# Performance work log

Measured on AMD Instinct MI355X. Metric: run time of the kernel, lower is better.

Reference implementation:

```python
import jax, jax.numpy as jnp
import numpy as np

WH, WW = 7, 7
N_HEADS = 6
INPUT_DIM = 192
HEAD_DIM = INPUT_DIM // N_HEADS
QK_SCALE = HEAD_DIM ** (-0.5)


def _relative_position_index(wh, ww):
    coords = np.stack(np.meshgrid(np.arange(wh), np.arange(ww), indexing='ij'))  # (2, wh, ww)
    cf = coords.reshape(2, -1)                       # (2, N)
    rel = cf[:, :, None] - cf[:, None, :]            # (2, N, N)
    rel = rel.transpose(1, 2, 0).copy()              # (N, N, 2)
    rel[:, :, 0] += wh - 1
    rel[:, :, 1] += ww - 1
    rel[:, :, 0] *= 2 * ww - 1
    return jnp.asarray(rel.sum(-1), dtype=jnp.int32)  # (N, N)

_REL_IDX = _relative_position_index(WH, WW)


def setup_inputs() -> dict:
    key = jax.random.key(0)
    ks = jax.random.split(key, 7)
    bW, nW = 4096, 64
    N = WH * WW
    s = 0.02
    return {
        "x": jax.random.normal(ks[0], (bW, WH, WW, INPUT_DIM), jnp.float32),
        "mask": jax.random.normal(ks[1], (nW, N, N), jnp.float32),
        "qkv_w": jax.random.normal(ks[2], (3 * INPUT_DIM, INPUT_DIM), jnp.float32) * s,
        "qkv_b": jax.random.normal(ks[3], (3 * INPUT_DIM,), jnp.float32) * s,
        "out_w": jax.random.normal(ks[4], (INPUT_DIM, INPUT_DIM), jnp.float32) * s,
        "out_b": jax.random.normal(ks[5], (INPUT_DIM,), jnp.float32) * s,
        "rpb_table": jax.random.normal(ks[6], ((2 * WH - 1) * (2 * WW - 1), N_HEADS), jnp.float32) * s,
    }


def reference(x, mask, qkv_w, qkv_b, out_w, out_b, rpb_table):
    b, Wh, Ww, C = x.shape
    N = Wh * Ww
    H, D = N_HEADS, HEAD_DIM
    # 1x1 conv == pointwise linear over channels-last input
    qkv = jnp.einsum('bxyc,oc->bxyo', x, qkv_w) + qkv_b          # (b, Wh, Ww, 3C)
    qkv = qkv.reshape(b, N, 3, H, D)                             # chunk order q,k,v; (h d) channel layout
    q, k, v = qkv[:, :, 0], qkv[:, :, 1], qkv[:, :, 2]           # (b, N, H, D)
    q = q * QK_SCALE
    sim = jnp.einsum('bihd,bjhd->bhij', q, k)                    # (b, H, N, N)
    # relative position bias gather
    rpb = rpb_table[_REL_IDX]                                    # (N, N, H)
    sim = sim + rpb.transpose(2, 0, 1)[None]                     # + (1, H, N, N)
    # shift mask add over windows
    nW = mask.shape[0]
    sim = sim.reshape(b // nW, nW, H, N, N) + mask[None, :, None]
    attn = jax.nn.softmax(sim, axis=-1).reshape(b, H, N, N)
    out = jnp.einsum('bhij,bjhd->bihd', attn, v)                 # (b, N, H, D)
    out = out.reshape(b, N, H * D)                               # (h d) channel order
    out = jnp.einsum('bnc,oc->bno', out, out_w) + out_b
    return out.reshape(b, Wh, Ww, C)
```

## Files before the change

### kernel.cpp

```cpp
#include <hip/hip_runtime.h>
#include <hip/hip_bf16.h>

typedef __bf16 bf16;
typedef __bf16 bf16x4 __attribute__((ext_vector_type(4)));
typedef __bf16 bf16x8 __attribute__((ext_vector_type(8)));
typedef float f32x4 __attribute__((ext_vector_type(4)));
typedef float floatv4 __attribute__((ext_vector_type(4)));

#define QK_SCALE 0.17677669529663687f

#define X_LD 200
#define QK_LD 40
#define VT_LD 72

__device__ __forceinline__ bf16* x_ptr(bf16* base, int row, int col) {
    return base + row * X_LD + col;
}
__device__ __forceinline__ bf16* qk_ptr(bf16* base, int row, int col) {
    return base + row * QK_LD + col;
}
__device__ __forceinline__ bf16* vt_ptr(bf16* base, int row, int col) {
    return base + row * VT_LD + col;
}

__global__ void wmsa_prep(const float* __restrict__ qkv_w,
                          const float* __restrict__ out_w,
                          const float* __restrict__ rpb_table,
                          const float* __restrict__ mask,
                          bf16* __restrict__ qkv_wb,
                          bf16* __restrict__ out_wb,
                          float* __restrict__ rpbx,
                          float* __restrict__ combo,
                          int build_combo) {
    int t = blockIdx.x * 256 + threadIdx.x;
    if (t < 110592) qkv_wb[t] = (bf16)qkv_w[t];
    if (t < 36864)  out_wb[t] = (bf16)out_w[t];
    if (t < 14406) {
        int h = t / 2401, ij = t % 2401, i = ij / 49, j = ij % 49;
        int ri = (i / 7 - j / 7 + 6) * 13 + (i % 7 - j % 7 + 6);
        rpbx[t] = rpb_table[ri * 6 + h];
    }
    if (build_combo && t < 64 * 6 * 64 * 64) {
        int j = t & 63, i = (t >> 6) & 63, r = t >> 12;
        int h = r % 6, w = r / 6;
        float v = -1e30f;
        if (i < 49 && j < 49) {
            int ri = (i / 7 - j / 7 + 6) * 13 + (i % 7 - j % 7 + 6);
            v = rpb_table[ri * 6 + h] + mask[w * 2401 + i * 49 + j];
        }
        combo[t] = v;
    }
}

template <bool USE_COMBO>
__global__ __launch_bounds__(768, 3) void wmsa_fused(
    const float* __restrict__ x, const float* __restrict__ mask,
    const float* __restrict__ qkv_b, const float* __restrict__ out_b,
    const bf16* __restrict__ qkv_wb, const bf16* __restrict__ out_wb,
    const float* __restrict__ rpbx, const float* __restrict__ combo,
    float* __restrict__ out)
{
    __shared__ __align__(16) bf16 s_x[64 * X_LD];
    __shared__ __align__(16) bf16 s_qp[6][64 * QK_LD];
    __shared__ __align__(16) bf16 s_k[6][64 * QK_LD];
    __shared__ __align__(16) bf16 s_vt[6][32 * VT_LD];

    const int b    = blockIdx.x;
    const int tid  = threadIdx.x;
    const int wv   = tid >> 6;
    const int lane = tid & 63;
    const int lo   = lane & 15;
    const int hi   = lane >> 4;

    const float* xw    = x + (size_t)b * 9408;
    const int    obase = wv * 48;
    const int    sec   = wv >> 2;

    {
        const int c0 = tid;
        const int r0s = c0 / 24, cc0 = c0 % 24;
        const float* p0 = xw + r0s * 192 + cc0 * 8;
        floatv4 f0 = *(const floatv4*)p0;
        floatv4 f1 = *(const floatv4*)(p0 + 4);
        bf16x8 v;
        v[0]=(bf16)f0[0]; v[1]=(bf16)f0[1]; v[2]=(bf16)f0[2]; v[3]=(bf16)f0[3];
        v[4]=(bf16)f1[0]; v[5]=(bf16)f1[1]; v[6]=(bf16)f1[2]; v[7]=(bf16)f1[3];
        *(bf16x8*)&s_x[r0s * X_LD + cc0 * 8] = v;

        const int c1 = tid + 768;
        const int r1s = c1 / 24, cc1 = c1 % 24;
        bf16x8 w = {};
        if (r1s < 49) {
            const float* p1 = xw + r1s * 192 + cc1 * 8;
            floatv4 g0 = *(const floatv4*)p1;
            floatv4 g1 = *(const floatv4*)(p1 + 4);
            w[0]=(bf16)g0[0]; w[1]=(bf16)g0[1]; w[2]=(bf16)g0[2]; w[3]=(bf16)g0[3];
            w[4]=(bf16)g1[0]; w[5]=(bf16)g1[1]; w[6]=(bf16)g1[2]; w[7]=(bf16)g1[3];
        }
        *(bf16x8*)&s_x[r1s * X_LD + cc1 * 8] = w;
    }
    __syncthreads();

#pragma unroll 1
    for (int mib = 0; mib < 2; ++mib) {
        f32x4 acc[2][3];
#pragma unroll
        for (int mi = 0; mi < 2; ++mi)
#pragma unroll
            for (int nj = 0; nj < 3; ++nj) acc[mi][nj] = (f32x4){0.f, 0.f, 0.f, 0.f};

        const int r0 = mib * 32 + lo;
        const int r1 = r0 + 16;

        auto loadB = [&](bf16x8* dst, int kk) {
#pragma unroll
            for (int nj = 0; nj < 3; ++nj)
                dst[nj] = *(const bf16x8*)(qkv_wb + (obase + nj * 16 + lo) * 192 + kk * 32 + hi * 8);
        };

        bf16x8 b0_[3], b1_[3], b2_[3];
        loadB(b0_, 0);
        loadB(b1_, 1);
#pragma unroll
        for (int kk = 0; kk < 6; ++kk) {
            if (kk < 4) loadB(b2_, kk + 2);
            bf16x8 a0 = *(const bf16x8*)x_ptr(s_x, r0, kk * 32 + hi * 8);
            bf16x8 a1 = *(const bf16x8*)x_ptr(s_x, r1, kk * 32 + hi * 8);
            acc[0][0] = __builtin_amdgcn_mfma_f32_16x16x32_bf16(a0, b0_[0], acc[0][0], 0, 0, 0);
            acc[1][0] = __builtin_amdgcn_mfma_f32_16x16x32_bf16(a1, b0_[0], acc[1][0], 0, 0, 0);
            acc[0][1] = __builtin_amdgcn_mfma_f32_16x16x32_bf16(a0, b0_[1], acc[0][1], 0, 0, 0);
            acc[1][1] = __builtin_amdgcn_mfma_f32_16x16x32_bf16(a1, b0_[1], acc[1][1], 0, 0, 0);
            acc[0][2] = __builtin_amdgcn_mfma_f32_16x16x32_bf16(a0, b0_[2], acc[0][2], 0, 0, 0);
            acc[1][2] = __builtin_amdgcn_mfma_f32_16x16x32_bf16(a1, b0_[2], acc[1][2], 0, 0, 0);
            b0_[0] = b1_[0]; b0_[1] = b1_[1]; b0_[2] = b1_[2];
            b1_[0] = b2_[0]; b1_[1] = b2_[1]; b1_[2] = b2_[2];
        }

        if (sec < 2) {
#pragma unroll
            for (int nj = 0; nj < 3; ++nj) {
                const int o    = obase + nj * 16 + lo;
                const float bs = qkv_b[o];
                const int oc   = o - sec * 192;
                const int hh   = oc >> 5;
                const int dd   = oc & 31;
                bf16* base = (sec == 0) ? &s_qp[hh][0] : &s_k[hh][0];
#pragma unroll
                for (int mi = 0; mi < 2; ++mi)
#pragma unroll
                    for (int r = 0; r < 4; ++r) {
                        const int n = mib * 32 + mi * 16 + hi * 4 + r;
                        const float v = acc[mi][nj][r] + bs;
                        *qk_ptr(base, n, dd) = (sec == 0) ? (bf16)(v * QK_SCALE) : (bf16)v;
                    }
            }
        } else {
#pragma unroll
            for (int nj = 0; nj < 3; ++nj) {
                const int o    = obase + nj * 16 + lo;
                const float bs = qkv_b[o];
                const int oc   = o - 384;
                const int hh   = oc >> 5;
                const int dd   = oc & 31;
#pragma unroll
                for (int mi = 0; mi < 2; ++mi) {
                    const int n0 = mib * 32 + mi * 16 + hi * 4;
                    bf16x4 pk;
#pragma unroll
                    for (int r = 0; r < 4; ++r) pk[r] = (bf16)(acc[mi][nj][r] + bs);
                    *(bf16x4*)vt_ptr(&s_vt[hh][0], dd, n0) = pk;
                }
            }
        }
    }
    __syncthreads();

    {
        const int h    = wv >> 1;
        const int arow = (wv & 1) * 32;
        bf16* qb    = &s_qp[h][0];
        bf16* kbase = &s_k[h][0];

        f32x4 cv[2][4];
        if (USE_COMBO) {
            const float* cb = combo + (((size_t)(b & 63) * 6 + h) << 12);
#pragma unroll
            for (int mi = 0; mi < 2; ++mi) {
                const int i = arow + mi * 16 + lo;
#pragma unroll
                for (int nt = 0; nt < 4; ++nt)
                    cv[mi][nt] = *(const floatv4*)(cb + i * 64 + nt * 16 + hi * 4);
            }
        }

        bf16x8 qa0 = *(const bf16x8*)qk_ptr(qb, arow + lo, hi * 8);
        bf16x8 qa1 = *(const bf16x8*)qk_ptr(qb, arow + 16 + lo, hi * 8);
        bf16x8 kb0 = *(const bf16x8*)qk_ptr(kbase,  0 + lo, hi * 8);
        bf16x8 kb1 = *(const bf16x8*)qk_ptr(kbase, 16 + lo, hi * 8);
        bf16x8 kb2 = *(const bf16x8*)qk_ptr(kbase, 32 + lo, hi * 8);
        bf16x8 kb3 = *(const bf16x8*)qk_ptr(kbase, 48 + lo, hi * 8);

        f32x4 t[4][2];
#pragma unroll
        for (int nt = 0; nt < 4; ++nt)
#pragma unroll
            for (int mi = 0; mi < 2; ++mi) t[nt][mi] = (f32x4){0.f, 0.f, 0.f, 0.f};
        t[0][0] = __builtin_amdgcn_mfma_f32_16x16x32_bf16(kb0, qa0, t[0][0], 0, 0, 0);
        t[1][0] = __builtin_amdgcn_mfma_f32_16x16x32_bf16(kb1, qa0, t[1][0], 0, 0, 0);
        t[2][0] = __builtin_amdgcn_mfma_f32_16x16x32_bf16(kb2, qa0, t[2][0], 0, 0, 0);
        t[3][0] = __builtin_amdgcn_mfma_f32_16x16x32_bf16(kb3, qa0, t[3][0], 0, 0, 0);
        t[0][1] = __builtin_amdgcn_mfma_f32_16x16x32_bf16(kb0, qa1, t[0][1], 0, 0, 0);
        t[1][1] = __builtin_amdgcn_mfma_f32_16x16x32_bf16(kb1, qa1, t[1][1], 0, 0, 0);
        t[2][1] = __builtin_amdgcn_mfma_f32_16x16x32_bf16(kb2, qa1, t[2][1], 0, 0, 0);
        t[3][1] = __builtin_amdgcn_mfma_f32_16x16x32_bf16(kb3, qa1, t[3][1], 0, 0, 0);

        if (USE_COMBO) {
#pragma unroll
            for (int mi = 0; mi < 2; ++mi)
#pragma unroll
                for (int nt = 0; nt < 4; ++nt) t[nt][mi] += cv[mi][nt];
        } else {
            const float* mk = mask + (size_t)(b & 63) * 2401;
            const float* rb = rpbx + h * 2401;
#pragma unroll
            for (int nt = 0; nt < 4; ++nt)
#pragma unroll
                for (int mi = 0; mi < 2; ++mi)
#pragma unroll
                    for (int r = 0; r < 4; ++r) {
                        const int i = arow + mi * 16 + lo;
                        const int j = nt * 16 + hi * 4 + r;
                        float sv = t[nt][mi][r];
                        if (j >= 49 || i >= 49) sv = -1e30f;
                        else sv += rb[i * 49 + j] + mk[i * 49 + j];
                        t[nt][mi][r] = sv;
                    }
        }

#pragma unroll
        for (int mi = 0; mi < 2; ++mi) {
            float m = t[0][mi][0];
#pragma unroll
            for (int nt = 0; nt < 4; ++nt)
#pragma unroll
                for (int r = 0; r < 4; ++r) m = fmaxf(m, t[nt][mi][r]);
            m = fmaxf(m, __shfl_xor(m, 16));
            m = fmaxf(m, __shfl_xor(m, 32));
            float sum = 0.f;
#pragma unroll
            for (int nt = 0; nt < 4; ++nt)
#pragma unroll
                for (int r = 0; r < 4; ++r) {
                    float pv = __expf(t[nt][mi][r] - m);
                    t[nt][mi][r] = pv;
                    sum += pv;
                }
            sum += __shfl_xor(sum, 16);
            sum += __shfl_xor(sum, 32);
            const float inv = 1.0f / sum;
#pragma unroll
            for (int nt = 0; nt < 4; ++nt)
#pragma unroll
                for (int r = 0; r < 4; ++r) t[nt][mi][r] *= inv;
        }

        f32x4 o00 = (f32x4){0.f,0.f,0.f,0.f}, o01 = (f32x4){0.f,0.f,0.f,0.f};
        f32x4 o10 = (f32x4){0.f,0.f,0.f,0.f}, o11 = (f32x4){0.f,0.f,0.f,0.f};
#pragma unroll
        for (int kk = 0; kk < 2; ++kk) {
#pragma unroll
            for (int mi = 0; mi < 2; ++mi)
#pragma unroll
                for (int c = 0; c < 2; ++c) {
                    const int nt = kk * 2 + c;
                    bf16x4 pk;
#pragma unroll
                    for (int r = 0; r < 4; ++r) pk[r] = (bf16)t[nt][mi][r];
                    *(bf16x4*)qk_ptr(qb, arow + mi * 16 + lo, c * 16 + hi * 4) = pk;
                }
            bf16x8 pa0 = *(const bf16x8*)qk_ptr(qb, arow + lo, hi * 8);
            bf16x8 pa1 = *(const bf16x8*)qk_ptr(qb, arow + 16 + lo, hi * 8);
            bf16x8 vb0 = *(const bf16x8*)vt_ptr(&s_vt[h][0],  0 + lo, kk * 32 + hi * 8);
            bf16x8 vb1 = *(const bf16x8*)vt_ptr(&s_vt[h][0], 16 + lo, kk * 32 + hi * 8);
            o00 = __builtin_amdgcn_mfma_f32_16x16x32_bf16(vb0, pa0, o00, 0, 0, 0);
            o01 = __builtin_amdgcn_mfma_f32_16x16x32_bf16(vb0, pa1, o01, 0, 0, 0);
            o10 = __builtin_amdgcn_mfma_f32_16x16x32_bf16(vb1, pa0, o10, 0, 0, 0);
            o11 = __builtin_amdgcn_mfma_f32_16x16x32_bf16(vb1, pa1, o11, 0, 0, 0);
        }

        {
            bf16x4 w00, w01, w10, w11;
#pragma unroll
            for (int r = 0; r < 4; ++r) {
                w00[r] = (bf16)o00[r]; w01[r] = (bf16)o01[r];
                w10[r] = (bf16)o10[r]; w11[r] = (bf16)o11[r];
            }
            *(bf16x4*)x_ptr(s_x, arow +  0 + lo, h * 32 +  0 + hi * 4) = w00;
            *(bf16x4*)x_ptr(s_x, arow + 16 + lo, h * 32 +  0 + hi * 4) = w01;
            *(bf16x4*)x_ptr(s_x, arow +  0 + lo, h * 32 + 16 + hi * 4) = w10;
            *(bf16x4*)x_ptr(s_x, arow + 16 + lo, h * 32 + 16 + hi * 4) = w11;
        }
    }
    __syncthreads();

    {
        const int o2 = wv * 16 + lo;
        f32x4 facc[4];
#pragma unroll
        for (int mi = 0; mi < 4; ++mi) facc[mi] = (f32x4){0.f, 0.f, 0.f, 0.f};

        bf16x8 fbc = *(const bf16x8*)(out_wb + o2 * 192 + hi * 8);
#pragma unroll
        for (int kk = 0; kk < 6; ++kk) {
            bf16x8 fbn;
            if (kk < 5) fbn = *(const bf16x8*)(out_wb + o2 * 192 + (kk + 1) * 32 + hi * 8);
            bf16x8 fa[4];
#pragma unroll
            for (int mi = 0; mi < 4; ++mi)
                fa[mi] = *(const bf16x8*)x_ptr(s_x, mi * 16 + lo, kk * 32 + hi * 8);
#pragma unroll
            for (int mi = 0; mi < 4; ++mi)
                facc[mi] = __builtin_amdgcn_mfma_f32_16x16x32_bf16(fa[mi], fbc, facc[mi], 0, 0, 0);
            fbc = fbn;
        }

        const float ob = out_b[o2];
        float* ow = out + (size_t)b * 9408;
#pragma unroll
        for (int mi = 0; mi < 4; ++mi)
#pragma unroll
            for (int r = 0; r < 4; ++r) {
                const int n = mi * 16 + hi * 4 + r;
                if (n < 49) ow[n * 192 + o2] = facc[mi][r] + ob;
            }
    }
}

extern "C" void kernel_launch(void* const* d_in, const int* in_sizes, int n_in,
                              void* d_out, int out_size, void* d_ws, size_t ws_size,
                              hipStream_t stream) {
    const float* x      = (const float*)d_in[0];
    const float* mask   = (const float*)d_in[1];
    const float* qkv_w  = (const float*)d_in[2];
    const float* qkv_b  = (const float*)d_in[3];
    const float* out_w  = (const float*)d_in[4];
    const float* out_b  = (const float*)d_in[5];
    const float* rpb    = (const float*)d_in[6];
    float* out          = (float*)d_out;

    char* ws = (char*)d_ws;
    bf16*  qkv_wb = (bf16*)ws;
    bf16*  out_wb = (bf16*)(ws + 221184);
    float* rpbx   = (float*)(ws + 294912);
    float* combo  = (float*)(ws + 352768);
    const bool use_combo = ws_size >= (size_t)(352768 + 6291456);

    hipLaunchKernelGGL(wmsa_prep, dim3(6144), dim3(256), 0, stream,
                       qkv_w, out_w, rpb, mask, qkv_wb, out_wb, rpbx, combo,
                       use_combo ? 1 : 0);
    if (use_combo)
        hipLaunchKernelGGL(HIP_KERNEL_NAME(wmsa_fused<true>), dim3(4096), dim3(768), 0, stream,
                           x, mask, qkv_b, out_b, qkv_wb, out_wb, rpbx, combo, out);
    else
        hipLaunchKernelGGL(HIP_KERNEL_NAME(wmsa_fused<false>), dim3(4096), dim3(768), 0, stream,
                           x, mask, qkv_b, out_b, qkv_wb, out_wb, rpbx, combo, out);
}
```

Measured before the change: 257.7 us.

## Halve block to 384 threads with compact swizzled LDS to fit more blocks

New measurement: 323.8 us. 1.26x slower.

```diff
diff --git a/kernel.cpp b/kernel.cpp
--- a/kernel.cpp
+++ b/kernel.cpp
@@ -9,18 +9,14 @@
 
 #define QK_SCALE 0.17677669529663687f
 
-#define X_LD 200
-#define QK_LD 40
-#define VT_LD 72
-
-__device__ __forceinline__ bf16* x_ptr(bf16* base, int row, int col) {
-    return base + row * X_LD + col;
+__device__ __forceinline__ bf16* t192_ptr(bf16* base, int row, int col) {
+    return base + row * 192 + ((((col >> 3) ^ (row & 7)) << 3)) + (col & 7);
 }
 __device__ __forceinline__ bf16* qk_ptr(bf16* base, int row, int col) {
-    return base + row * QK_LD + col;
+    return base + row * 32 + ((((col >> 3) ^ ((row >> 1) & 3)) << 3)) + (col & 7);
 }
 __device__ __forceinline__ bf16* vt_ptr(bf16* base, int row, int col) {
-    return base + row * VT_LD + col;
+    return base + row * 56 + col;
 }
 
 __global__ void wmsa_prep(const float* __restrict__ qkv_w,
@@ -53,17 +49,18 @@
 }
 
 template <bool USE_COMBO>
-__global__ __launch_bounds__(768, 3) void wmsa_fused(
+__global__ __launch_bounds__(384, 3) void wmsa_fused(
     const float* __restrict__ x, const float* __restrict__ mask,
     const float* __restrict__ qkv_b, const float* __restrict__ out_b,
     const bf16* __restrict__ qkv_wb, const bf16* __restrict__ out_wb,
     const float* __restrict__ rpbx, const float* __restrict__ combo,
     float* __restrict__ out)
 {
-    __shared__ __align__(16) bf16 s_x[64 * X_LD];
-    __shared__ __align__(16) bf16 s_qp[6][64 * QK_LD];
-    __shared__ __align__(16) bf16 s_k[6][64 * QK_LD];
-    __shared__ __align__(16) bf16 s_vt[6][32 * VT_LD];
+    __shared__ __align__(16) bf16 s_lds[39360];
+    bf16* s_x  = s_lds;
+    bf16* s_q  = s_lds + 9408;
+    bf16* s_k  = s_lds + 19008;
+    bf16* s_vt = s_lds + 28608;
 
     const int b    = blockIdx.x;
     const int tid  = threadIdx.x;
@@ -72,239 +69,247 @@
     const int lo   = lane & 15;
     const int hi   = lane >> 4;
 
-    const float* xw    = x + (size_t)b * 9408;
-    const int    obase = wv * 48;
-    const int    sec   = wv >> 2;
+    const float* xw  = x + (size_t)b * 9408;
+    const int    sec = wv >> 1;
+
+#pragma unroll
+    for (int q2 = 0; q2 < 4; ++q2) {
+        const int gc = q2 * 384 + tid;
+        if (gc < 1176) {
+            const int rs = gc / 24, cc = gc % 24;
+            const float* p = xw + rs * 192 + cc * 8;
+            floatv4 f0 = *(const floatv4*)p;
+            floatv4 f1 = *(const floatv4*)(p + 4);
+            bf16x8 v;
+            v[0]=(bf16)f0[0]; v[1]=(bf16)f0[1]; v[2]=(bf16)f0[2]; v[3]=(bf16)f0[3];
+            v[4]=(bf16)f1[0]; v[5]=(bf16)f1[1]; v[6]=(bf16)f1[2]; v[7]=(bf16)f1[3];
+            *(bf16x8*)&s_x[(rs * 24 + (cc ^ (rs & 7))) * 8] = v;
+        }
+    }
+    __syncthreads();
+
+#pragma unroll 1
+    for (int nj2 = 0; nj2 < 2; ++nj2) {
+        const int colbase = wv * 96 + nj2 * 48;
+#pragma unroll 1
+        for (int mib = 0; mib < 2; ++mib) {
+            f32x4 acc[2][3];
+#pragma unroll
+            for (int mi = 0; mi < 2; ++mi)
+#pragma unroll
+                for (int nj = 0; nj < 3; ++nj) acc[mi][nj] = (f32x4){0.f, 0.f, 0.f, 0.f};
+
+            const int r0 = mib * 32 + lo;
+            const int r1 = min(r0 + 16, 48);
+
+            auto loadB = [&](bf16x8* dst, int kk) {
+#pragma unroll
+                for (int nj = 0; nj < 3; ++nj)
+                    dst[nj] = *(const bf16x8*)(qkv_wb + (colbase + nj * 16 + lo) * 192 + kk * 32 + hi * 8);
+            };
+
+            bf16x8 b0_[3], b1_[3], b2_[3];
+            loadB(b0_, 0);
+            loadB(b1_, 1);
+#pragma unroll
+            for (int kk = 0; kk < 6; ++kk) {
+                if (kk < 4) loadB(b2_, kk + 2);
+                bf16x8 a0 = *(const bf16x8*)t192_ptr(s_x, r0, kk * 32 + hi * 8);
+                bf16x8 a1 = *(const bf16x8*)t192_ptr(s_x, r1, kk * 32 + hi * 8);
+                acc[0][0] = __builtin_amdgcn_mfma_f32_16x16x32_bf16(a0, b0_[0], acc[0][0], 0, 0, 0);
+                acc[1][0] = __builtin_amdgcn_mfma_f32_16x16x32_bf16(a1, b0_[0], acc[1][0], 0, 0, 0);
+                acc[0][1] = __builtin_amdgcn_mfma_f32_16x16x32_bf16(a0, b0_[1], acc[0][1], 0, 0, 0);
+                acc[1][1] = __builtin_amdgcn_mfma_f32_16x16x32_bf16(a1, b0_[1], acc[1][1], 0, 0, 0);
+                acc[0][2] = __builtin_amdgcn_mfma_f32_16x16x32_bf16(a0, b0_[2], acc[0][2], 0, 0, 0);
+                acc[1][2] = __builtin_amdgcn_mfma_f32_16x16x32_bf16(a1, b0_[2], acc[1][2], 0, 0, 0);
+                b0_[0] = b1_[0]; b0_[1] = b1_[1]; b0_[2] = b1_[2];
+                b1_[0] = b2_[0]; b1_[1] = b2_[1]; b1_[2] = b2_[2];
+            }
+
+            if (sec < 2) {
+#pragma unroll
+                for (int nj = 0; nj < 3; ++nj) {
+                    const int o    = colbase + nj * 16 + lo;
+                    const float bs = qkv_b[o];
+                    const int oc   = o - sec * 192;
+                    const int hh   = oc >> 5;
+                    const int dd   = oc & 31;
+                    bf16* base = (sec == 0) ? (s_q + hh * 1600) : (s_k + hh * 1600);
+#pragma unroll
+                    for (int mi = 0; mi < 2; ++mi)
+#pragma unroll
+                        for (int r = 0; r < 4; ++r) {
+                            const int n  = mib * 32 + mi * 16 + hi * 4 + r;
+                            const int nc = min(n, 49);
+                            const float v = acc[mi][nj][r] + bs;
+                            *qk_ptr(base, nc, dd) = (sec == 0) ? (bf16)(v * QK_SCALE) : (bf16)v;
+                        }
+                }
+            } else {
+#pragma unroll
+                for (int nj = 0; nj < 3; ++nj) {
+                    const int o    = colbase + nj * 16 + lo;
+                    const float bs = qkv_b[o];
+                    const int oc   = o - 384;
+                    const int hh   = oc >> 5;
+                    const int dd   = oc & 31;
+#pragma unroll
+                    for (int mi = 0; mi < 2; ++mi) {
+                        const int n0 = mib * 32 + mi * 16 + hi * 4;
+                        if (n0 < 56) {
+                            bf16x4 pk;
+#pragma unroll
+                            for (int r = 0; r < 4; ++r) pk[r] = (bf16)(acc[mi][nj][r] + bs);
+                            *(bf16x4*)vt_ptr(s_vt + hh * 1792, dd, n0) = pk;
+                        }
+                    }
+                }
+            }
+        }
+    }
+    __syncthreads();
 
     {
-        const int c0 = tid;
-        const int r0s = c0 / 24, cc0 = c0 % 24;
-        const float* p0 = xw + r0s * 192 + cc0 * 8;
-        floatv4 f0 = *(const floatv4*)p0;
-        floatv4 f1 = *(const floatv4*)(p0 + 4);
-        bf16x8 v;
-        v[0]=(bf16)f0[0]; v[1]=(bf16)f0[1]; v[2]=(bf16)f0[2]; v[3]=(bf16)f0[3];
-        v[4]=(bf16)f1[0]; v[5]=(bf16)f1[1]; v[6]=(bf16)f1[2]; v[7]=(bf16)f1[3];
-        *(bf16x8*)&s_x[r0s * X_LD + cc0 * 8] = v;
-
-        const int c1 = tid + 768;
-        const int r1s = c1 / 24, cc1 = c1 % 24;
-        bf16x8 w = {};
-        if (r1s < 49) {
-            const float* p1 = xw + r1s * 192 + cc1 * 8;
-            floatv4 g0 = *(const floatv4*)p1;
-            floatv4 g1 = *(const floatv4*)(p1 + 4);
-            w[0]=(bf16)g0[0]; w[1]=(bf16)g0[1]; w[2]=(bf16)g0[2]; w[3]=(bf16)g0[3];
-            w[4]=(bf16)g1[0]; w[5]=(bf16)g1[1]; w[6]=(bf16)g1[2]; w[7]=(bf16)g1[3];
-        }
-        *(bf16x8*)&s_x[r1s * X_LD + cc1 * 8] = w;
+        const int h = wv;
+        bf16* qb    = s_q + h * 1600;
+        bf16* kbase = s_k + h * 1600;
+        bf16* vtb   = s_vt + h * 1792;
+
+#pragma unroll 1
+        for (int p = 0; p < 2; ++p) {
+            const int arow = p * 32;
+
+            f32x4 cv[2][4];
+            if (USE_COMBO) {
+                const float* cb = combo + (((size_t)(b & 63) * 6 + h) << 12);
+#pragma unroll
+                for (int mi = 0; mi < 2; ++mi) {
+                    const int i = arow + mi * 16 + lo;
+#pragma unroll
+                    for (int nt = 0; nt < 4; ++nt)
+                        cv[mi][nt] = *(const floatv4*)(cb + i * 64 + nt * 16 + hi * 4);
+                }
+            }
+
+            bf16x8 qa0 = *(const bf16x8*)qk_ptr(qb, arow + lo, hi * 8);
+            bf16x8 qa1 = *(const bf16x8*)qk_ptr(qb, min(arow + 16 + lo, 49), hi * 8);
+            bf16x8 kb0 = *(const bf16x8*)qk_ptr(kbase,  0 + lo, hi * 8);
+            bf16x8 kb1 = *(const bf16x8*)qk_ptr(kbase, 16 + lo, hi * 8);
+            bf16x8 kb2 = *(const bf16x8*)qk_ptr(kbase, 32 + lo, hi * 8);
+            bf16x8 kb3 = *(const bf16x8*)qk_ptr(kbase, min(48 + lo, 49), hi * 8);
+
+            f32x4 t[4][2];
+#pragma unroll
+            for (int nt = 0; nt < 4; ++nt)
+#pragma unroll
+                for (int mi = 0; mi < 2; ++mi) t[nt][mi] = (f32x4){0.f, 0.f, 0.f, 0.f};
+            t[0][0] = __builtin_amdgcn_mfma_f32_16x16x32_bf16(kb0, qa0, t[0][0], 0, 0, 0);
+            t[1][0] = __builtin_amdgcn_mfma_f32_16x16x32_bf16(kb1, qa0, t[1][0], 0, 0, 0);
+            t[2][0] = __builtin_amdgcn_mfma_f32_16x16x32_bf16(kb2, qa0, t[2][0], 0, 0, 0);
+            t[3][0] = __builtin_amdgcn_mfma_f32_16x16x32_bf16(kb3, qa0, t[3][0], 0, 0, 0);
+            t[0][1] = __builtin_amdgcn_mfma_f32_16x16x32_bf16(kb0, qa1, t[0][1], 0, 0, 0);
+            t[1][1] = __builtin_amdgcn_mfma_f32_16x16x32_bf16(kb1, qa1, t[1][1], 0, 0, 0);
+            t[2][1] = __builtin_amdgcn_mfma_f32_16x16x32_bf16(kb2, qa1, t[2][1], 0, 0, 0);
+            t[3][1] = __builtin_amdgcn_mfma_f32_16x16x32_bf16(kb3, qa1, t[3][1], 0, 0, 0);
+
+            if (USE_COMBO) {
+#pragma unroll
+                for (int mi = 0; mi < 2; ++mi)
+#pragma unroll
+                    for (int nt = 0; nt < 4; ++nt) t[nt][mi] += cv[mi][nt];
+            } else {
+                const float* mk = mask + (size_t)(b & 63) * 2401;
+                const float* rb = rpbx + h * 2401;
+#pragma unroll
+                for (int nt = 0; nt < 4; ++nt)
+#pragma unroll
+                    for (int mi = 0; mi < 2; ++mi)
+#pragma unroll
+                        for (int r = 0; r < 4; ++r) {
+                            const int i = arow + mi * 16 + lo;
+                            const int j = nt * 16 + hi * 4 + r;
+                            float sv = t[nt][mi][r];
+                            if (j >= 49 || i >= 49) sv = -1e30f;
+                            else sv += rb[i * 49 + j] + mk[i * 49 + j];
+                            t[nt][mi][r] = sv;
+                        }
+            }
+
+#pragma unroll
+            for (int mi = 0; mi < 2; ++mi) {
+                float m = t[0][mi][0];
+#pragma unroll
+                for (int nt = 0; nt < 4; ++nt)
+#pragma unroll
+                    for (int r = 0; r < 4; ++r) m = fmaxf(m, t[nt][mi][r]);
+                m = fmaxf(m, __shfl_xor(m, 16));
+                m = fmaxf(m, __shfl_xor(m, 32));
+                float sum = 0.f;
+#pragma unroll
+                for (int nt = 0; nt < 4; ++nt)
+#pragma unroll
+                    for (int r = 0; r < 4; ++r) {
+                        float pv = __expf(t[nt][mi][r] - m);
+                        t[nt][mi][r] = pv;
+                        sum += pv;
+                    }
+                sum += __shfl_xor(sum, 16);
+                sum += __shfl_xor(sum, 32);
+                const float inv = 1.0f / sum;
+#pragma unroll
+                for (int nt = 0; nt < 4; ++nt)
+#pragma unroll
+                    for (int r = 0; r < 4; ++r) t[nt][mi][r] *= inv;
+            }
+
+            f32x4 o00 = (f32x4){0.f,0.f,0.f,0.f}, o01 = (f32x4){0.f,0.f,0.f,0.f};
+            f32x4 o10 = (f32x4){0.f,0.f,0.f,0.f}, o11 = (f32x4){0.f,0.f,0.f,0.f};
+#pragma unroll
+            for (int kk = 0; kk < 2; ++kk) {
+#pragma unroll
+                for (int mi = 0; mi < 2; ++mi)
+#pragma unroll
+                    for (int c = 0; c < 2; ++c) {
+                        const int nt = kk * 2 + c;
+                        bf16x4 pk;
+#pragma unroll
+                        for (int r = 0; r < 4; ++r) pk[r] = (bf16)t[nt][mi][r];
+                        *(bf16x4*)qk_ptr(qb, min(arow + mi * 16 + lo, 49), c * 16 + hi * 4) = pk;
+                    }
+                bf16x8 pa0 = *(const bf16x8*)qk_ptr(qb, arow + lo, hi * 8);
+                bf16x8 pa1 = *(const bf16x8*)qk_ptr(qb, min(arow + 16 + lo, 49), hi * 8);
+                const int vc = min(kk * 32 + hi * 8, 48);
+                bf16x8 vb0 = *(const bf16x8*)vt_ptr(vtb,  0 + lo, vc);
+                bf16x8 vb1 = *(const bf16x8*)vt_ptr(vtb, 16 + lo, vc);
+                o00 = __builtin_amdgcn_mfma_f32_16x16x32_bf16(vb0, pa0, o00, 0, 0, 0);
+                o01 = __builtin_amdgcn_mfma_f32_16x16x32_bf16(vb0, pa1, o01, 0, 0, 0);
+                o10 = __builtin_amdgcn_mfma_f32_16x16x32_bf16(vb1, pa0, o10, 0, 0, 0);
+                o11 = __builtin_amdgcn_mfma_f32_16x16x32_bf16(vb1, pa1, o11, 0, 0, 0);
+            }
+
+            {
+                bf16x4 w00, w01, w10, w11;
+#pragma unroll
+                for (int r = 0; r < 4; ++r) {
+                    w00[r] = (bf16)o00[r]; w01[r] = (bf16)o01[r];
+                    w10[r] = (bf16)o10[r]; w11[r] = (bf16)o11[r];
+                }
+                const int row0 = arow + lo;
+                const int row1 = arow + 16 + lo;
+                *(bf16x4*)t192_ptr(s_x, row0, h * 32 +  0 + hi * 4) = w00;
+                *(bf16x4*)t192_ptr(s_x, row0, h * 32 + 16 + hi * 4) = w10;
+                if (row1 < 49) {
+                    *(bf16x4*)t192_ptr(s_x, row1, h * 32 +  0 + hi * 4) = w01;
+                    *(bf16x4*)t192_ptr(s_x, row1, h * 32 + 16 + hi * 4) = w11;
+                }
+            }
+        }
     }
     __syncthreads();
 
 #pragma unroll 1
-    for (int mib = 0; mib < 2; ++mib) {
-        f32x4 acc[2][3];
-#pragma unroll
-        for (int mi = 0; mi < 2; ++mi)
-#pragma unroll
-            for (int nj = 0; nj < 3; ++nj) acc[mi][nj] = (f32x4){0.f, 0.f, 0.f, 0.f};
-
-        const int r0 = mib * 32 + lo;
-        const int r1 = r0 + 16;
-
-        auto loadB = [&](bf16x8* dst, int kk) {
-#pragma unroll
-            for (int nj = 0; nj < 3; ++nj)
-                dst[nj] = *(const bf16x8*)(qkv_wb + (obase + nj * 16 + lo) * 192 + kk * 32 + hi * 8);
-        };
-
-        bf16x8 b0_[3], b1_[3], b2_[3];
-        loadB(b0_, 0);
-        loadB(b1_, 1);
-#pragma unroll
-        for (int kk = 0; kk < 6; ++kk) {
-            if (kk < 4) loadB(b2_, kk + 2);
-            bf16x8 a0 = *(const bf16x8*)x_ptr(s_x, r0, kk * 32 + hi * 8);
-            bf16x8 a1 = *(const bf16x8*)x_ptr(s_x, r1, kk * 32 + hi * 8);
-            acc[0][0] = __builtin_amdgcn_mfma_f32_16x16x32_bf16(a0, b0_[0], acc[0][0], 0, 0, 0);
-            acc[1][0] = __builtin_amdgcn_mfma_f32_16x16x32_bf16(a1, b0_[0], acc[1][0], 0, 0, 0);
-            acc[0][1] = __builtin_amdgcn_mfma_f32_16x16x32_bf16(a0, b0_[1], acc[0][1], 0, 0, 0);
-            acc[1][1] = __builtin_amdgcn_mfma_f32_16x16x32_bf16(a1, b0_[1], acc[1][1], 0, 0, 0);
-            acc[0][2] = __builtin_amdgcn_mfma_f32_16x16x32_bf16(a0, b0_[2], acc[0][2], 0, 0, 0);
-            acc[1][2] = __builtin_amdgcn_mfma_f32_16x16x32_bf16(a1, b0_[2], acc[1][2], 0, 0, 0);
-            b0_[0] = b1_[0]; b0_[1] = b1_[1]; b0_[2] = b1_[2];
-            b1_[0] = b2_[0]; b1_[1] = b2_[1]; b1_[2] = b2_[2];
-        }
-
-        if (sec < 2) {
-#pragma unroll
-            for (int nj = 0; nj < 3; ++nj) {
-                const int o    = obase + nj * 16 + lo;
-                const float bs = qkv_b[o];
-                const int oc   = o - sec * 192;
-                const int hh   = oc >> 5;
-                const int dd   = oc & 31;
-                bf16* base = (sec == 0) ? &s_qp[hh][0] : &s_k[hh][0];
-#pragma unroll
-                for (int mi = 0; mi < 2; ++mi)
-#pragma unroll
-                    for (int r = 0; r < 4; ++r) {
-                        const int n = mib * 32 + mi * 16 + hi * 4 + r;
-                        const float v = acc[mi][nj][r] + bs;
-                        *qk_ptr(base, n, dd) = (sec == 0) ? (bf16)(v * QK_SCALE) : (bf16)v;
-                    }
-            }
-        } else {
-#pragma unroll
-            for (int nj = 0; nj < 3; ++nj) {
-                const int o    = obase + nj * 16 + lo;
-                const float bs = qkv_b[o];
-                const int oc   = o - 384;
-                const int hh   = oc >> 5;
-                const int dd   = oc & 31;
-#pragma unroll
-                for (int mi = 0; mi < 2; ++mi) {
-                    const int n0 = mib * 32 + mi * 16 + hi * 4;
-                    bf16x4 pk;
-#pragma unroll
-                    for (int r = 0; r < 4; ++r) pk[r] = (bf16)(acc[mi][nj][r] + bs);
-                    *(bf16x4*)vt_ptr(&s_vt[hh][0], dd, n0) = pk;
-                }
-            }
-        }
-    }
-    __syncthreads();
-
-    {
-        const int h    = wv >> 1;
-        const int arow = (wv & 1) * 32;
-        bf16* qb    = &s_qp[h][0];
-        bf16* kbase = &s_k[h][0];
-
-        f32x4 cv[2][4];
-        if (USE_COMBO) {
-            const float* cb = combo + (((size_t)(b & 63) * 6 + h) << 12);
-#pragma unroll
-            for (int mi = 0; mi < 2; ++mi) {
-                const int i = arow + mi * 16 + lo;
-#pragma unroll
-                for (int nt = 0; nt < 4; ++nt)
-                    cv[mi][nt] = *(const floatv4*)(cb + i * 64 + nt * 16 + hi * 4);
-            }
-        }
-
-        bf16x8 qa0 = *(const bf16x8*)qk_ptr(qb, arow + lo, hi * 8);
-        bf16x8 qa1 = *(const bf16x8*)qk_ptr(qb, arow + 16 + lo, hi * 8);
-        bf16x8 kb0 = *(const bf16x8*)qk_ptr(kbase,  0 + lo, hi * 8);
-        bf16x8 kb1 = *(const bf16x8*)qk_ptr(kbase, 16 + lo, hi * 8);
-        bf16x8 kb2 = *(const bf16x8*)qk_ptr(kbase, 32 + lo, hi * 8);
-        bf16x8 kb3 = *(const bf16x8*)qk_ptr(kbase, 48 + lo, hi * 8);
-
-        f32x4 t[4][2];
-#pragma unroll
-        for (int nt = 0; nt < 4; ++nt)
-#pragma unroll
-            for (int mi = 0; mi < 2; ++mi) t[nt][mi] = (f32x4){0.f, 0.f, 0.f, 0.f};
-        t[0][0] = __builtin_amdgcn_mfma_f32_16x16x32_bf16(kb0, qa0, t[0][0], 0, 0, 0);
-        t[1][0] = __builtin_amdgcn_mfma_f32_16x16x32_bf16(kb1, qa0, t[1][0], 0, 0, 0);
-        t[2][0] = __builtin_amdgcn_mfma_f32_16x16x32_bf16(kb2, qa0, t[2][0], 0, 0, 0);
-        t[3][0] = __builtin_amdgcn_mfma_f32_16x16x32_bf16(kb3, qa0, t[3][0], 0, 0, 0);
-        t[0][1] = __builtin_amdgcn_mfma_f32_16x16x32_bf16(kb0, qa1, t[0][1], 0, 0, 0);
-        t[1][1] = __builtin_amdgcn_mfma_f32_16x16x32_bf16(kb1, qa1, t[1][1], 0, 0, 0);
-        t[2][1] = __builtin_amdgcn_mfma_f32_16x16x32_bf16(kb2, qa1, t[2][1], 0, 0, 0);
-        t[3][1] = __builtin_amdgcn_mfma_f32_16x16x32_bf16(kb3, qa1, t[3][1], 0, 0, 0);
-
-        if (USE_COMBO) {
-#pragma unroll
-            for (int mi = 0; mi < 2; ++mi)
-#pragma unroll
-                for (int nt = 0; nt < 4; ++nt) t[nt][mi] += cv[mi][nt];
-        } else {
-            const float* mk = mask + (size_t)(b & 63) * 2401;
-            const float* rb = rpbx + h * 2401;
-#pragma unroll
-            for (int nt = 0; nt < 4; ++nt)
-#pragma unroll
-                for (int mi = 0; mi < 2; ++mi)
-#pragma unroll
-                    for (int r = 0; r < 4; ++r) {
-                        const int i = arow + mi * 16 + lo;
-                        const int j = nt * 16 + hi * 4 + r;
-                        float sv = t[nt][mi][r];
-                        if (j >= 49 || i >= 49) sv = -1e30f;
-                        else sv += rb[i * 49 + j] + mk[i * 49 + j];
-                        t[nt][mi][r] = sv;
-                    }
-        }
-
-#pragma unroll
-        for (int mi = 0; mi < 2; ++mi) {
-            float m = t[0][mi][0];
-#pragma unroll
-            for (int nt = 0; nt < 4; ++nt)
-#pragma unroll
-                for (int r = 0; r < 4; ++r) m = fmaxf(m, t[nt][mi][r]);
-            m = fmaxf(m, __shfl_xor(m, 16));
-            m = fmaxf(m, __shfl_xor(m, 32));
-            float sum = 0.f;
-#pragma unroll
-            for (int nt = 0; nt < 4; ++nt)
-#pragma unroll
-                for (int r = 0; r < 4; ++r) {
-                    float pv = __expf(t[nt][mi][r] - m);
-                    t[nt][mi][r] = pv;
-                    sum += pv;
-                }
-            sum += __shfl_xor(sum, 16);
-            sum += __shfl_xor(sum, 32);
-            const float inv = 1.0f / sum;
-#pragma unroll
-            for (int nt = 0; nt < 4; ++nt)
-#pragma unroll
-                for (int r = 0; r < 4; ++r) t[nt][mi][r] *= inv;
-        }
-
-        f32x4 o00 = (f32x4){0.f,0.f,0.f,0.f}, o01 = (f32x4){0.f,0.f,0.f,0.f};
-        f32x4 o10 = (f32x4){0.f,0.f,0.f,0.f}, o11 = (f32x4){0.f,0.f,0.f,0.f};
-#pragma unroll
-        for (int kk = 0; kk < 2; ++kk) {
-#pragma unroll
-            for (int mi = 0; mi < 2; ++mi)
-#pragma unroll
-                for (int c = 0; c < 2; ++c) {
-                    const int nt = kk * 2 + c;
-                    bf16x4 pk;
-#pragma unroll
-                    for (int r = 0; r < 4; ++r) pk[r] = (bf16)t[nt][mi][r];
-                    *(bf16x4*)qk_ptr(qb, arow + mi * 16 + lo, c * 16 + hi * 4) = pk;
-                }
-            bf16x8 pa0 = *(const bf16x8*)qk_ptr(qb, arow + lo, hi * 8);
-            bf16x8 pa1 = *(const bf16x8*)qk_ptr(qb, arow + 16 + lo, hi * 8);
-            bf16x8 vb0 = *(const bf16x8*)vt_ptr(&s_vt[h][0],  0 + lo, kk * 32 + hi * 8);
-            bf16x8 vb1 = *(const bf16x8*)vt_ptr(&s_vt[h][0], 16 + lo, kk * 32 + hi * 8);
-            o00 = __builtin_amdgcn_mfma_f32_16x16x32_bf16(vb0, pa0, o00, 0, 0, 0);
-            o01 = __builtin_amdgcn_mfma_f32_16x16x32_bf16(vb0, pa1, o01, 0, 0, 0);
-            o10 = __builtin_amdgcn_mfma_f32_16x16x32_bf16(vb1, pa0, o10, 0, 0, 0);
-            o11 = __builtin_amdgcn_mfma_f32_16x16x32_bf16(vb1, pa1, o11, 0, 0, 0);
-        }
-
-        {
-            bf16x4 w00, w01, w10, w11;
-#pragma unroll
-            for (int r = 0; r < 4; ++r) {
-                w00[r] = (bf16)o00[r]; w01[r] = (bf16)o01[r];
-                w10[r] = (bf16)o10[r]; w11[r] = (bf16)o11[r];
-            }
-            *(bf16x4*)x_ptr(s_x, arow +  0 + lo, h * 32 +  0 + hi * 4) = w00;
-            *(bf16x4*)x_ptr(s_x, arow + 16 + lo, h * 32 +  0 + hi * 4) = w01;
-            *(bf16x4*)x_ptr(s_x, arow +  0 + lo, h * 32 + 16 + hi * 4) = w10;
-            *(bf16x4*)x_ptr(s_x, arow + 16 + lo, h * 32 + 16 + hi * 4) = w11;
-        }
-    }
-    __syncthreads();
-
-    {
-        const int o2 = wv * 16 + lo;
+    for (int t2 = 0; t2 < 2; ++t2) {
+        const int o2 = wv * 32 + t2 * 16 + lo;
         f32x4 facc[4];
 #pragma unroll
         for (int mi = 0; mi < 4; ++mi) facc[mi] = (f32x4){0.f, 0.f, 0.f, 0.f};
@@ -317,7 +322,7 @@
             bf16x8 fa[4];
 #pragma unroll
             for (int mi = 0; mi < 4; ++mi)
-                fa[mi] = *(const bf16x8*)x_ptr(s_x, mi * 16 + lo, kk * 32 + hi * 8);
+                fa[mi] = *(const bf16x8*)t192_ptr(s_x, mi * 16 + lo, kk * 32 + hi * 8);
 #pragma unroll
             for (int mi = 0; mi < 4; ++mi)
                 facc[mi] = __builtin_amdgcn_mfma_f32_16x16x32_bf16(fa[mi], fbc, facc[mi], 0, 0, 0);
@@ -359,9 +364,9 @@
                        qkv_w, out_w, rpb, mask, qkv_wb, out_wb, rpbx, combo,
                        use_combo ? 1 : 0);
     if (use_combo)
-        hipLaunchKernelGGL(HIP_KERNEL_NAME(wmsa_fused<true>), dim3(4096), dim3(768), 0, stream,
+        hipLaunchKernelGGL(HIP_KERNEL_NAME(wmsa_fused<true>), dim3(4096), dim3(384), 0, stream,
                            x, mask, qkv_b, out_b, qkv_wb, out_wb, rpbx, combo, out);
     else
-        hipLaunchKernelGGL(HIP_KERNEL_NAME(wmsa_fused<false>), dim3(4096), dim3(768), 0, stream,
+        hipLaunchKernelGGL(HIP_KERNEL_NAME(wmsa_fused<false>), dim3(4096), dim3(384), 0, stream,
                            x, mask, qkv_b, out_b, qkv_wb, out_wb, rpbx, combo, out);
 }
```
